# Optimization experiments

Measured on AMD Instinct MI355X. Metric: run time of the kernel, lower is better.

The kernel has to match this reference:

```python
import jax, jax.numpy as jnp
import numpy as np


def _graph_conv_mean(x, src, dst, edge_weight, W_rel, W_root, b, num_nodes):
    # messages: gather source features, optionally scale by edge weight
    msg = x[src]  # [E, D]
    if edge_weight is not None:
        msg = msg * edge_weight[:, None]
    # mean aggregation over incoming edges per destination node
    summed = jax.ops.segment_sum(msg, dst, num_segments=num_nodes)  # [N, D]
    count = jax.ops.segment_sum(jnp.ones((src.shape[0],), x.dtype), dst, num_segments=num_nodes)
    mean = summed / jnp.maximum(count, 1.0)[:, None]
    # out = lin_rel(mean) + lin_root(x) + bias
    return mean @ W_rel + x @ W_root + b


def setup_inputs() -> dict:
    key = jax.random.key(0)
    ks = jax.random.split(key, 8)
    N, E, D, H, C = 100000, 1600000, 128, 32, 5
    x = jax.random.normal(ks[0], (N, D), dtype=jnp.float32)
    edge_index = jax.random.randint(ks[1], (2, E), 0, N, dtype=jnp.int64)
    edge_weight = jax.random.uniform(ks[2], (E,), dtype=jnp.float32)
    W_rel1 = jax.random.normal(ks[3], (D, H), dtype=jnp.float32) / np.sqrt(D)
    W_root1 = jax.random.normal(ks[4], (D, H), dtype=jnp.float32) / np.sqrt(D)
    b1 = jnp.zeros((H,), jnp.float32)
    W_rel2 = jax.random.normal(ks[5], (H, C), dtype=jnp.float32) / np.sqrt(H)
    W_root2 = jax.random.normal(ks[6], (H, C), dtype=jnp.float32) / np.sqrt(H)
    b2 = jnp.zeros((C,), jnp.float32)
    return {"x": x, "edge_index": edge_index, "edge_weight": edge_weight,
            "W_rel1": W_rel1, "W_root1": W_root1, "b1": b1,
            "W_rel2": W_rel2, "W_root2": W_root2, "b2": b2}


def reference(x, edge_index, edge_weight, W_rel1, W_root1, b1, W_rel2, W_root2, b2):
    N = x.shape[0]
    src, dst = edge_index[0], edge_index[1]
    # conv1 with edge_weight
    h = _graph_conv_mean(x, src, dst, edge_weight, W_rel1, W_root1, b1, N)
    h = jax.nn.relu(h)
    # dropout is identity at inference (training=False)
    # conv2 without edge_weight
    out = _graph_conv_mean(h, src, dst, None, W_rel2, W_root2, b2, N)
    return jax.nn.log_softmax(out, axis=1)
```

## Files before the change

### kernel.cpp

```cpp
#include <hip/hip_runtime.h>
#include <math.h>

#define N_NODES 100000
#define E_EDGES 1600000
#define D_IN    128
#define H_MID   32
#define C_OUT   5

#define BSHIFT 8
#define BNODES 256
#define NBKT   391
#define BCAP   4500
#define SRC_BITS 17
#define SRC_MASK 0x1FFFF

#define EB     2048
#define NBA    782
#define NMF    1563

#define KP 136

typedef __attribute__((ext_vector_type(8))) short bf16x8;
typedef __attribute__((ext_vector_type(4))) float f32x4;

__device__ inline unsigned f2bf(float f) {
    unsigned u = __float_as_uint(f);
    return (u + 0x7FFFu + ((u >> 16) & 1u)) >> 16;
}
__device__ inline float bflo(unsigned v) { return __uint_as_float((v & 0xFFFFu) << 16); }
__device__ inline float bfhi(unsigned v) { return __uint_as_float(v & 0xFFFF0000u); }
__device__ inline float bf2f(unsigned short u) { return __uint_as_float(((unsigned)u) << 16); }

__global__ void k_prep(const float* __restrict__ Wrel,
                       const float* __restrict__ Wroot,
                       int* __restrict__ bucket_cursor,
                       unsigned short* __restrict__ wt_g) {
    int tid = threadIdx.x;
    bucket_cursor[tid] = 0;
    for (int i = tid; i < 64 * 128; i += 512) {
        int n = i >> 7, k = i & 127;
        float v = (n < H_MID) ? Wrel[k * H_MID + n] : Wroot[k * H_MID + (n - H_MID)];
        wt_g[i] = (unsigned short)f2bf(v);
    }
}

__global__ __launch_bounds__(512) void k_front(
    const int* __restrict__ src,
    const int* __restrict__ dst,
    const float* __restrict__ ew,
    int* __restrict__ bucket_cursor,
    int2* __restrict__ staged,
    const float* __restrict__ x,
    const unsigned short* __restrict__ wt_g,
    const float* __restrict__ b1,
    unsigned short* __restrict__ xrelh,
    float* __restrict__ xroot) {
    __shared__ __align__(16) char smem[26752];
    int tid = threadIdx.x;

    if (blockIdx.x < NBA) {
        int2*  ebuf   = (int2*)smem;
        short* bbuf   = (short*)(smem + 16384);
        int*   cnt0   = (int*)(smem + 20480);
        int*   cnt1   = (int*)(smem + 22044);
        int*   lstart = (int*)(smem + 23608);
        int*   gbase  = (int*)(smem + 25172);
        int*   totp   = (int*)(smem + 26736);
        int eBase = blockIdx.x * EB;
        int half = tid >> 8;
        int* cntH = half ? cnt1 : cnt0;

        if (tid < NBKT) { cnt0[tid] = 0; cnt1[tid] = 0; }
        __syncthreads();

        int b[4], rank[4], packed[4], wbits[4];
        bool valid[4];
        #pragma unroll
        for (int u = 0; u < 4; ++u) {
            int e = eBase + u * 512 + tid;
            valid[u] = (e < E_EDGES);
            b[u] = 0; rank[u] = 0; packed[u] = 0; wbits[u] = 0;
            if (valid[u]) {
                int d = dst[e];
                int s = src[e];
                wbits[u] = __float_as_int(ew[e]);
                b[u] = d >> BSHIFT;
                packed[u] = ((d & (BNODES - 1)) << SRC_BITS) | s;
                rank[u] = atomicAdd(&cntH[b[u]], 1);
            }
        }
        __syncthreads();

        if (tid < 64) {
            int base = tid * 7;
            int loc[7];
            int s = 0;
            #pragma unroll
            for (int k = 0; k < 7; ++k) {
                int idx = base + k;
                int c = (idx < NBKT) ? (cnt0[idx] + cnt1[idx]) : 0;
                loc[k] = s;
                s += c;
            }
            int run = s;
            #pragma unroll
            for (int off = 1; off < 64; off <<= 1) {
                int t = __shfl_up(run, off, 64);
                if (tid >= off) run += t;
            }
            int excl = run - s;
            #pragma unroll
            for (int k = 0; k < 7; ++k) {
                int idx = base + k;
                if (idx < NBKT) lstart[idx] = excl + loc[k];
            }
            if (tid == 63) *totp = run;
        }
        if (tid < NBKT)
            gbase[tid] = atomicAdd(&bucket_cursor[tid], cnt0[tid] + cnt1[tid]);
        __syncthreads();
        int total = *totp;

        #pragma unroll
        for (int u = 0; u < 4; ++u) {
            if (valid[u]) {
                int rg = rank[u] + (half ? cnt0[b[u]] : 0);
                int slot = lstart[b[u]] + rg;
                ebuf[slot] = make_int2(packed[u], wbits[u]);
                bbuf[slot] = (short)b[u];
            }
        }
        __syncthreads();

        for (int t = tid; t < total; t += 512) {
            int2 ev = ebuf[t];
            int bb = bbuf[t];
            int gpos = gbase[bb] + (t - lstart[bb]);
            if (gpos < BCAP)
                staged[(size_t)bb * BCAP + gpos] = ev;
        }
    } else {
        unsigned short* xs = (unsigned short*)smem;
        int nodeBase = (blockIdx.x - NBA) * 64;

        #pragma unroll
        for (int it = 0; it < 8; ++it) {
            int idx = it * 512 + tid;
            int row = idx >> 6, kp = idx & 63;
            int node = nodeBase + row;
            float2 v = make_float2(0.f, 0.f);
            if (node < N_NODES)
                v = *(const float2*)(x + (size_t)node * D_IN + kp * 2);
            unsigned pk = f2bf(v.x) | (f2bf(v.y) << 16);
            *(unsigned*)(xs + row * KP + kp * 2) = pk;
        }
        __syncthreads();

        int lane = tid & 63;
        int wv = tid >> 6;
        int m = lane & 15;
        int quad = lane >> 4;
        int rowBase = (wv & 3) * 16;
        int ntBase = (wv >> 2) * 2;

        f32x4 acc[2];
        acc[0] = (f32x4){0.f, 0.f, 0.f, 0.f};
        acc[1] = (f32x4){0.f, 0.f, 0.f, 0.f};

        #pragma unroll
        for (int kk = 0; kk < 4; ++kk) {
            int k0 = kk * 32 + quad * 8;
            bf16x8 a = *(const bf16x8*)(xs + (rowBase + m) * KP + k0);
            #pragma unroll
            for (int t = 0; t < 2; ++t) {
                bf16x8 bb = *(const bf16x8*)(wt_g + ((ntBase + t) * 16 + m) * 128 + k0);
                acc[t] = __builtin_amdgcn_mfma_f32_16x16x32_bf16(a, bb, acc[t], 0, 0, 0);
            }
        }

        #pragma unroll
        for (int t = 0; t < 2; ++t) {
            #pragma unroll
            for (int r = 0; r < 4; ++r) {
                int node = nodeBase + rowBase + quad * 4 + r;
                int colg = (ntBase + t) * 16 + m;
                if (node < N_NODES) {
                    if (colg < H_MID) {
                        xrelh[(size_t)node * H_MID + colg] =
                            (unsigned short)f2bf(acc[t][r]);
                    } else {
                        int c = colg - H_MID;
                        xroot[(size_t)node * H_MID + c] = acc[t][r] + b1[c];
                    }
                }
            }
        }
    }
}

__global__ __launch_bounds__(1024) void k_bucket1(
    const int* __restrict__ bucket_cursor,
    const int2* __restrict__ staged,
    const unsigned short* __restrict__ xrelh,
    const float* __restrict__ xroot,
    const float* __restrict__ Wrel2,
    const float* __restrict__ Wroot2,
    const float* __restrict__ b2,
    unsigned short* __restrict__ h2rel8,
    float* __restrict__ h2root,
    int* __restrict__ csr_srcb,
    int* __restrict__ deg_g,
    int* __restrict__ nst_g) {
    __shared__ int2 ecsr[BCAP];
    __shared__ int hist0[BNODES];
    __shared__ int hist1[BNODES];
    __shared__ int nstart[BNODES];
    __shared__ int cur0[BNODES];
    __shared__ int cur1[BNODES];
    int tid = threadIdx.x;
    int b = blockIdx.x;
    int half = tid >> 9;
    int* histH = half ? hist1 : hist0;
    int* curH  = half ? cur1  : cur0;

    int count = bucket_cursor[b];
    if (count > BCAP) count = BCAP;
    const int2* sp = staged + (size_t)b * BCAP;

    if (tid < BNODES) { hist0[tid] = 0; hist1[tid] = 0; }
    __syncthreads();
    for (int i = tid; i < count; i += 1024)
        atomicAdd(&histH[((unsigned)sp[i].x) >> SRC_BITS], 1);
    __syncthreads();

    if (tid < 64) {
        int base = tid * 4;
        int loc[4];
        int s = 0;
        #pragma unroll
        for (int k = 0; k < 4; ++k) {
            loc[k] = s;
            s += hist0[base + k] + hist1[base + k];
        }
        int run = s;
        #pragma unroll
        for (int off = 1; off < 64; off <<= 1) {
            int t = __shfl_up(run, off, 64);
            if (tid >= off) run += t;
        }
        int excl = run - s;
        #pragma unroll
        for (int k = 0; k < 4; ++k)
            nstart[base + k] = excl + loc[k];
    }
    __syncthreads();
    if (tid < BNODES) {
        int h0 = hist0[tid];
        cur0[tid] = nstart[tid];
        cur1[tid] = nstart[tid] + h0;
        int node = b * BNODES + tid;
        if (node < N_NODES) {
            deg_g[node] = h0 + hist1[tid];
            nst_g[node] = nstart[tid];
        }
    }
    __syncthreads();

    for (int i = tid; i < count; i += 1024) {
        int2 ev = sp[i];
        int local = ((unsigned)ev.x) >> SRC_BITS;
        int pos = atomicAdd(&curH[local], 1);
        ecsr[pos] = make_int2(ev.x & SRC_MASK, ev.y);
    }
    __syncthreads();

    int* outb = csr_srcb + (size_t)b * BCAP;
    for (int i = tid; i < count; i += 1024)
        outb[i] = ecsr[i].x;

    int g = tid >> 4;
    int lane = tid & 15;
    for (int nl = g; nl < BNODES; nl += 64) {
        int node = b * BNODES + nl;
        if (node >= N_NODES) continue;
        int dg = hist0[nl] + hist1[nl];
        int i = nstart[nl];
        int end = i + dg;

        float acc0 = 0.f, acc1 = 0.f;
        for (; i + 8 <= end; i += 8) {
            int2 e[8];
            unsigned v[8];
            #pragma unroll
            for (int u = 0; u < 8; ++u) e[u] = ecsr[i + u];
            #pragma unroll
            for (int u = 0; u < 8; ++u)
                v[u] = *(const unsigned*)(xrelh + (size_t)e[u].x * H_MID + lane * 2);
            #pragma unroll
            for (int u = 0; u < 8; ++u) {
                float w = __int_as_float(e[u].y);
                acc0 += bflo(v[u]) * w;
                acc1 += bfhi(v[u]) * w;
            }
        }
        for (; i < end; ++i) {
            int2 e0 = ecsr[i];
            unsigned v0 = *(const unsigned*)(xrelh + (size_t)e0.x * H_MID + lane * 2);
            float w0 = __int_as_float(e0.y);
            acc0 += bflo(v0) * w0;
            acc1 += bfhi(v0) * w0;
        }

        float inv = 1.0f / fmaxf((float)dg, 1.0f);
        float2 rt = *(const float2*)(xroot + (size_t)node * H_MID + lane * 2);
        float h0 = fmaxf(acc0 * inv + rt.x, 0.f);
        float h1 = fmaxf(acc1 * inv + rt.y, 0.f);

        float p[2 * C_OUT];
        #pragma unroll
        for (int j = 0; j < C_OUT; ++j) {
            p[j]         = h0 * Wrel2[(2 * lane) * C_OUT + j]
                         + h1 * Wrel2[(2 * lane + 1) * C_OUT + j];
            p[C_OUT + j] = h0 * Wroot2[(2 * lane) * C_OUT + j]
                         + h1 * Wroot2[(2 * lane + 1) * C_OUT + j];
        }
        #pragma unroll
        for (int mm = 8; mm > 0; mm >>= 1) {
            #pragma unroll
            for (int j = 0; j < 2 * C_OUT; ++j)
                p[j] += __shfl_xor(p[j], mm, 16);
        }
        if (lane == 0) {
            #pragma unroll
            for (int j = 0; j < C_OUT; ++j) {
                h2rel8[(size_t)node * 8 + j] = (unsigned short)f2bf(p[j]);
                h2root[(size_t)node * C_OUT + j] = p[C_OUT + j] + b2[j];
            }
        }
    }
}

__global__ __launch_bounds__(256) void k_bucket2(
    const int* __restrict__ deg_g,
    const int* __restrict__ nst_g,
    const int* __restrict__ csr_srcb,
    const unsigned short* __restrict__ h2rel8,
    const float* __restrict__ h2root,
    float* __restrict__ out) {
    int node = blockIdx.x * 32 + (threadIdx.x >> 3);
    int lane = threadIdx.x & 7;
    int dg  = deg_g[node];
    int beg = (node >> BSHIFT) * BCAP + nst_g[node];
    int end = beg + dg;

    float acc = 0.f;
    if (lane < C_OUT) {
        int i = beg;
        int nfull = dg >> 3;
        if (nfull) {
            int s[8];
            #pragma unroll
            for (int u = 0; u < 8; ++u) s[u] = csr_srcb[i + u];
            for (int bb = 1; bb < nfull; ++bb) {
                float v[8];
                #pragma unroll
                for (int u = 0; u < 8; ++u)
                    v[u] = bf2f(h2rel8[(size_t)s[u] * 8 + lane]);
                int s2[8];
                #pragma unroll
                for (int u = 0; u < 8; ++u) s2[u] = csr_srcb[i + 8 + u];
                #pragma unroll
                for (int u = 0; u < 8; ++u) acc += v[u];
                #pragma unroll
                for (int u = 0; u < 8; ++u) s[u] = s2[u];
                i += 8;
            }
            #pragma unroll
            for (int u = 0; u < 8; ++u)
                acc += bf2f(h2rel8[(size_t)s[u] * 8 + lane]);
            i += 8;
        }
        for (; i < end; ++i)
            acc += bf2f(h2rel8[(size_t)csr_srcb[i] * 8 + lane]);
    }
    float inv = 1.0f / fmaxf((float)dg, 1.0f);
    float o = (lane < C_OUT)
                  ? acc * inv + h2root[(size_t)node * C_OUT + lane]
                  : -INFINITY;
    float m = o;
    #pragma unroll
    for (int dd = 4; dd > 0; dd >>= 1) m = fmaxf(m, __shfl_xor(m, dd, 8));
    float e = (lane < C_OUT) ? expf(o - m) : 0.f;
    float ssum = e;
    #pragma unroll
    for (int dd = 4; dd > 0; dd >>= 1) ssum += __shfl_xor(ssum, dd, 8);
    float lse = m + logf(ssum);
    if (lane < C_OUT)
        out[(size_t)node * C_OUT + lane] = o - lse;
}

extern "C" void kernel_launch(void* const* d_in, const int* in_sizes, int n_in,
                              void* d_out, int out_size, void* d_ws, size_t ws_size,
                              hipStream_t stream) {
    const float* x      = (const float*)d_in[0];
    const int*   ei     = (const int*)d_in[1];
    const float* ew     = (const float*)d_in[2];
    const float* Wrel1  = (const float*)d_in[3];
    const float* Wroot1 = (const float*)d_in[4];
    const float* b1     = (const float*)d_in[5];
    const float* Wrel2  = (const float*)d_in[6];
    const float* Wroot2 = (const float*)d_in[7];
    const float* b2     = (const float*)d_in[8];
    float* out = (float*)d_out;

    const int* src = ei;
    const int* dst = ei + E_EDGES;

    char* ws = (char*)d_ws;
    int*   bucket_cursor = (int*)ws;
    unsigned short* wt_g = (unsigned short*)(bucket_cursor + 512);
    int2*  staged        = (int2*)(wt_g + 64 * 128);
    unsigned short* xrelh = (unsigned short*)(staged + (size_t)NBKT * BCAP);
    float* xroot         = (float*)(xrelh + (size_t)N_NODES * H_MID);
    unsigned short* h2rel8 = (unsigned short*)(xroot + (size_t)N_NODES * H_MID);
    float* h2root        = (float*)(h2rel8 + (size_t)N_NODES * 8);
    int*   csr_srcb      = (int*)(h2root + (size_t)N_NODES * C_OUT);
    int*   deg_g         = csr_srcb + (size_t)NBKT * BCAP;
    int*   nst_g         = deg_g + N_NODES;

    k_prep<<<1, 512, 0, stream>>>(Wrel1, Wroot1, bucket_cursor, wt_g);

    k_front<<<NBA + NMF, 512, 0, stream>>>(src, dst, ew, bucket_cursor, staged,
                                           x, wt_g, b1, xrelh, xroot);

    k_bucket1<<<NBKT, 1024, 0, stream>>>(bucket_cursor, staged,
                                         xrelh, xroot, Wrel2, Wroot2, b2,
                                         h2rel8, h2root, csr_srcb, deg_g, nst_g);

    k_bucket2<<<N_NODES / 32, 256, 0, stream>>>(deg_g, nst_g, csr_srcb,
                                                h2rel8, h2root, out);
}
```

Measured before the change: 203.7 us.

## Drop weight-prep kernel, convert weights in-block, and double k_front block size

Removes the single-block k_prep launch: bucket cursors are now cleared with hipMemsetAsync, and each MFMA block converts W_rel1/W_root1 to bf16 into LDS itself. k_front blocks grow to 1024 threads, covering 4096 edges or 128 nodes each, which halves the block count and doubles shared memory per block. This cuts one dependent launch and keeps weight reads in LDS, at the cost of every MFMA block redoing the weight conversion and of lower occupancy from the larger LDS footprint.

Result: faster. 196.5 us, median of 2 (-3.5%).

```diff
diff --git a/kernel.cpp b/kernel.cpp
--- a/kernel.cpp
+++ b/kernel.cpp
@@ -14,9 +14,9 @@
 #define SRC_BITS 17
 #define SRC_MASK 0x1FFFF
 
-#define EB     2048
-#define NBA    782
-#define NMF    1563
+#define EB     4096
+#define NBA    391
+#define NMF    782
 
 #define KP 136
 
@@ -31,43 +31,31 @@
 __device__ inline float bfhi(unsigned v) { return __uint_as_float(v & 0xFFFF0000u); }
 __device__ inline float bf2f(unsigned short u) { return __uint_as_float(((unsigned)u) << 16); }
 
-__global__ void k_prep(const float* __restrict__ Wrel,
-                       const float* __restrict__ Wroot,
-                       int* __restrict__ bucket_cursor,
-                       unsigned short* __restrict__ wt_g) {
-    int tid = threadIdx.x;
-    bucket_cursor[tid] = 0;
-    for (int i = tid; i < 64 * 128; i += 512) {
-        int n = i >> 7, k = i & 127;
-        float v = (n < H_MID) ? Wrel[k * H_MID + n] : Wroot[k * H_MID + (n - H_MID)];
-        wt_g[i] = (unsigned short)f2bf(v);
-    }
-}
-
-__global__ __launch_bounds__(512) void k_front(
+__global__ __launch_bounds__(1024) void k_front(
     const int* __restrict__ src,
     const int* __restrict__ dst,
     const float* __restrict__ ew,
     int* __restrict__ bucket_cursor,
     int2* __restrict__ staged,
     const float* __restrict__ x,
-    const unsigned short* __restrict__ wt_g,
+    const float* __restrict__ Wrel1,
+    const float* __restrict__ Wroot1,
     const float* __restrict__ b1,
     unsigned short* __restrict__ xrelh,
     float* __restrict__ xroot) {
-    __shared__ __align__(16) char smem[26752];
+    __shared__ __align__(16) char smem[52224];
     int tid = threadIdx.x;
 
     if (blockIdx.x < NBA) {
         int2*  ebuf   = (int2*)smem;
-        short* bbuf   = (short*)(smem + 16384);
-        int*   cnt0   = (int*)(smem + 20480);
-        int*   cnt1   = (int*)(smem + 22044);
-        int*   lstart = (int*)(smem + 23608);
-        int*   gbase  = (int*)(smem + 25172);
-        int*   totp   = (int*)(smem + 26736);
+        short* bbuf   = (short*)(smem + 32768);
+        int*   cnt0   = (int*)(smem + 40960);
+        int*   cnt1   = (int*)(smem + 42524);
+        int*   lstart = (int*)(smem + 44088);
+        int*   gbase  = (int*)(smem + 45652);
+        int*   totp   = (int*)(smem + 47216);
         int eBase = blockIdx.x * EB;
-        int half = tid >> 8;
+        int half = tid >> 9;
         int* cntH = half ? cnt1 : cnt0;
 
         if (tid < NBKT) { cnt0[tid] = 0; cnt1[tid] = 0; }
@@ -77,7 +65,7 @@
         bool valid[4];
         #pragma unroll
         for (int u = 0; u < 4; ++u) {
-            int e = eBase + u * 512 + tid;
+            int e = eBase + u * 1024 + tid;
             valid[u] = (e < E_EDGES);
             b[u] = 0; rank[u] = 0; packed[u] = 0; wbits[u] = 0;
             if (valid[u]) {
@@ -132,7 +120,7 @@
         }
         __syncthreads();
 
-        for (int t = tid; t < total; t += 512) {
+        for (int t = tid; t < total; t += 1024) {
             int2 ev = ebuf[t];
             int bb = bbuf[t];
             int gpos = gbase[bb] + (t - lstart[bb]);
@@ -140,12 +128,13 @@
                 staged[(size_t)bb * BCAP + gpos] = ev;
         }
     } else {
-        unsigned short* xs = (unsigned short*)smem;
-        int nodeBase = (blockIdx.x - NBA) * 64;
+        unsigned short* xs   = (unsigned short*)smem;
+        unsigned short* wt_l = (unsigned short*)(smem + 34816);
+        int nodeBase = (blockIdx.x - NBA) * 128;
 
         #pragma unroll
         for (int it = 0; it < 8; ++it) {
-            int idx = it * 512 + tid;
+            int idx = it * 1024 + tid;
             int row = idx >> 6, kp = idx & 63;
             int node = nodeBase + row;
             float2 v = make_float2(0.f, 0.f);
@@ -154,14 +143,22 @@
             unsigned pk = f2bf(v.x) | (f2bf(v.y) << 16);
             *(unsigned*)(xs + row * KP + kp * 2) = pk;
         }
+        #pragma unroll
+        for (int it = 0; it < 8; ++it) {
+            int i = it * 1024 + tid;
+            int n = i >> 7, k = i & 127;
+            float v = (n < H_MID) ? Wrel1[k * H_MID + n]
+                                  : Wroot1[k * H_MID + (n - H_MID)];
+            wt_l[n * KP + k] = (unsigned short)f2bf(v);
+        }
         __syncthreads();
 
         int lane = tid & 63;
         int wv = tid >> 6;
         int m = lane & 15;
         int quad = lane >> 4;
-        int rowBase = (wv & 3) * 16;
-        int ntBase = (wv >> 2) * 2;
+        int rowBase = (wv & 7) * 16;
+        int ntBase = (wv >> 3) * 2;
 
         f32x4 acc[2];
         acc[0] = (f32x4){0.f, 0.f, 0.f, 0.f};
@@ -173,7 +170,7 @@
             bf16x8 a = *(const bf16x8*)(xs + (rowBase + m) * KP + k0);
             #pragma unroll
             for (int t = 0; t < 2; ++t) {
-                bf16x8 bb = *(const bf16x8*)(wt_g + ((ntBase + t) * 16 + m) * 128 + k0);
+                bf16x8 bb = *(const bf16x8*)(wt_l + ((ntBase + t) * 16 + m) * KP + k0);
                 acc[t] = __builtin_amdgcn_mfma_f32_16x16x32_bf16(a, bb, acc[t], 0, 0, 0);
             }
         }
@@ -418,8 +415,7 @@
 
     char* ws = (char*)d_ws;
     int*   bucket_cursor = (int*)ws;
-    unsigned short* wt_g = (unsigned short*)(bucket_cursor + 512);
-    int2*  staged        = (int2*)(wt_g + 64 * 128);
+    int2*  staged        = (int2*)(bucket_cursor + 512);
     unsigned short* xrelh = (unsigned short*)(staged + (size_t)NBKT * BCAP);
     float* xroot         = (float*)(xrelh + (size_t)N_NODES * H_MID);
     unsigned short* h2rel8 = (unsigned short*)(xroot + (size_t)N_NODES * H_MID);
@@ -428,10 +424,11 @@
     int*   deg_g         = csr_srcb + (size_t)NBKT * BCAP;
     int*   nst_g         = deg_g + N_NODES;
 
-    k_prep<<<1, 512, 0, stream>>>(Wrel1, Wroot1, bucket_cursor, wt_g);
-
-    k_front<<<NBA + NMF, 512, 0, stream>>>(src, dst, ew, bucket_cursor, staged,
-                                           x, wt_g, b1, xrelh, xroot);
+    hipMemsetAsync(bucket_cursor, 0, 512 * sizeof(int), stream);
+
+    k_front<<<NBA + NMF, 1024, 0, stream>>>(src, dst, ew, bucket_cursor,
+                                            staged, x, Wrel1, Wroot1, b1,
+                                            xrelh, xroot);
 
     k_bucket1<<<NBKT, 1024, 0, stream>>>(bucket_cursor, staged,
                                          xrelh, xroot, Wrel2, Wroot2, b2,
```
